# Kernel tuning notes

Hardware: AMD Instinct MI355X
Metric: run time of the kernel (lower is better)

## Reference

```python
import jax, jax.numpy as jnp
import numpy as np


def setup_inputs() -> dict:
    key = jax.random.key(0)
    B, T, D, H = 32, 2048, 128, 256
    ks = jax.random.split(key, 13)
    s_in = 1.0 / np.sqrt(D)
    s_h = 1.0 / np.sqrt(H)
    return {
        "x": jax.random.normal(ks[0], (B, T, D), jnp.float32),
        "wf": jax.random.normal(ks[1], (D, H), jnp.float32) * s_in,
        "wi": jax.random.normal(ks[2], (D, H), jnp.float32) * s_in,
        "wo": jax.random.normal(ks[3], (D, H), jnp.float32) * s_in,
        "wc": jax.random.normal(ks[4], (D, H), jnp.float32) * s_in,
        "uf": jax.random.normal(ks[5], (H, H), jnp.float32) * s_h,
        "ui": jax.random.normal(ks[6], (H, H), jnp.float32) * s_h,
        "uo": jax.random.normal(ks[7], (H, H), jnp.float32) * s_h,
        "uc": jax.random.normal(ks[8], (H, H), jnp.float32) * s_h,
        "bf": jax.random.normal(ks[9], (1, H), jnp.float32) * 0.01,
        "bi": jax.random.normal(ks[10], (1, H), jnp.float32) * 0.01,
        "bo": jax.random.normal(ks[11], (1, H), jnp.float32) * 0.01,
        "bc": jax.random.normal(ks[12], (1, H), jnp.float32) * 0.01,
    }


def reference(x, wf, wi, wo, wc, uf, ui, uo, uc, bf, bi, bo, bc):
    # Standard 4-gate LSTM over time, matching the per-gate weights of myLSTM.
    # Fuse the four input projections into one GEMM over all timesteps up front
    # (same math as per-step x_t @ w*), then scan the recurrence.
    B, T, D = x.shape
    H = wf.shape[1]
    W = jnp.concatenate([wf, wi, wo, wc], axis=1)            # [D, 4H]
    U = jnp.concatenate([uf, ui, uo, uc], axis=1)            # [H, 4H]
    b = jnp.concatenate([bf, bi, bo, bc], axis=1)            # [1, 4H]
    xg = jnp.einsum('btd,dg->btg', x, W) + b                 # [B, T, 4H]
    xg = jnp.swapaxes(xg, 0, 1)                              # [T, B, 4H]

    def step(carry, xg_t):
        h, c = carry
        g = xg_t + h @ U                                     # [B, 4H]
        f = jax.nn.sigmoid(g[:, 0 * H:1 * H])
        i = jax.nn.sigmoid(g[:, 1 * H:2 * H])
        o = jax.nn.sigmoid(g[:, 2 * H:3 * H])
        cand = jnp.tanh(g[:, 3 * H:4 * H])
        c_new = f * c + i * cand
        h_new = o * jnp.tanh(c_new)
        return (h_new, c_new), h_new

    h0 = jnp.zeros((B, H), x.dtype)
    c0 = jnp.zeros((B, H), x.dtype)
    (_, _), hs = jax.lax.scan(step, (h0, c0), xg)            # hs: [T, B, H]
    return jnp.swapaxes(hs, 0, 1)                            # [B, T, H]
```

## Files before the change

### kernel.cpp

```cpp
#include <hip/hip_runtime.h>
#include <hip/hip_fp16.h>
#include <cstdint>

#define BB 32
#define TT 2048
#define DD 128
#define HH 256

typedef _Float16 half2v __attribute__((ext_vector_type(2)));
typedef uint32_t u32x4 __attribute__((ext_vector_type(4)));

__device__ inline float dot2f16(uint32_t a, uint32_t b, float c) {
#if __has_builtin(__builtin_amdgcn_fdot2)
  half2v ah = __builtin_bit_cast(half2v, a);
  half2v bh = __builtin_bit_cast(half2v, b);
  return __builtin_amdgcn_fdot2(ah, bh, c, false);
#else
  float d;
  asm("v_dot2_f32_f16 %0, %1, %2, %3" : "=v"(d) : "v"(a), "v"(b), "v"(c));
  return d;
#endif
}

__device__ inline float fsigmoid(float x) { return __frcp_rn(1.f + __expf(-x)); }
__device__ inline float ftanh_(float x)   { return 1.f - 2.f * __frcp_rn(1.f + __expf(2.f * x)); }


__global__ void repack_u3_kernel(const float* __restrict__ uf, const float* __restrict__ ui_,
                                 const float* __restrict__ uo, const float* __restrict__ uc,
                                 __half* __restrict__ Ut) {
  int idx = blockIdx.x * 256 + threadIdx.x;
  int cg = idx >> 12;
  int rem = idx & 4095;
  int j = rem >> 3, r = rem & 7;
  int a = cg >> 3, c = cg & 7;
  int nn = a >> 2, g = a & 3;
  int s = j & 3, u = j >> 2;
  int n = 2 * u + nn;
  int k = s * 64 + c * 8 + r;
  const float* U[4] = {uf, ui_, uo, uc};
  Ut[idx] = __float2half(U[g][k * HH + n]);
}

__global__ void repack_w2_kernel(const float* __restrict__ wf, const float* __restrict__ wi,
                                 const float* __restrict__ wo, const float* __restrict__ wc,
                                 const float* __restrict__ bf, const float* __restrict__ bi,
                                 const float* __restrict__ bo, const float* __restrict__ bc,
                                 __half* __restrict__ Wt, float* __restrict__ bs) {
  int idx = blockIdx.x * 256 + threadIdx.x;
  int m = idx >> 7, k = idx & 127;
  int g = m & 3, n = m >> 2;
  const float* W[4] = {wf, wi, wo, wc};
  Wt[idx] = __float2half(W[g][k * HH + n]);
  if (idx < 1024) {
    const float* B[4] = {bf, bi, bo, bc};
    bs[idx] = B[idx & 3][idx >> 2];
  }
}

__global__ __launch_bounds__(256, 4) void xg_gemm_kernel(
    const float* __restrict__ x, const __half* __restrict__ Wt,
    const float* __restrict__ bs, __half* __restrict__ xg) {
  __shared__ __align__(16) __half As[64][136];
  __shared__ __align__(16) __half Bs[64][136];
  const int tid = threadIdx.x;
  const int r0 = (blockIdx.x >> 4) * 64;
  const int m0 = (blockIdx.x & 15) * 64;

#pragma unroll
  for (int it = 0; it < 8; ++it) {
    int fi = it * 256 + tid;
    int row = fi >> 5, col4 = fi & 31;
    float4 v = ((const float4*)(x + (size_t)(r0 + row) * DD))[col4];
    __half2 lo; lo.x = __float2half(v.x); lo.y = __float2half(v.y);
    __half2 hi; hi.x = __float2half(v.z); hi.y = __float2half(v.w);
    uint2 pk; pk.x = __builtin_bit_cast(uint32_t, lo); pk.y = __builtin_bit_cast(uint32_t, hi);
    *(uint2*)&As[row][col4 * 4] = pk;
  }
#pragma unroll
  for (int it = 0; it < 4; ++it) {
    int ui = it * 256 + tid;
    int row = ui >> 4, c16 = ui & 15;
    uint4 v = ((const uint4*)(Wt + (size_t)(m0 + row) * DD))[c16];
    *(uint4*)&Bs[row][c16 * 8] = v;
  }
  __syncthreads();

  const int ty = tid >> 4, tx = tid & 15;
  float acc[4][4] = {};
#pragma unroll
  for (int kc = 0; kc < 16; ++kc) {
    uint4 av[4], bv[4];
#pragma unroll
    for (int d = 0; d < 4; ++d) {
      av[d] = *(const uint4*)&As[ty * 4 + d][kc * 8];
      bv[d] = *(const uint4*)&Bs[tx * 4 + d][kc * 8];
    }
#pragma unroll
    for (int di = 0; di < 4; ++di)
#pragma unroll
      for (int dj = 0; dj < 4; ++dj) {
        acc[di][dj] = dot2f16(av[di].x, bv[dj].x, acc[di][dj]);
        acc[di][dj] = dot2f16(av[di].y, bv[dj].y, acc[di][dj]);
        acc[di][dj] = dot2f16(av[di].z, bv[dj].z, acc[di][dj]);
        acc[di][dj] = dot2f16(av[di].w, bv[dj].w, acc[di][dj]);
      }
  }

#pragma unroll
  for (int di = 0; di < 4; ++di) {
    const int grow = r0 + ty * 4 + di;
    __half2 o01, o23;
    o01.x = __float2half(acc[di][0] + bs[m0 + tx * 4 + 0]);
    o01.y = __float2half(acc[di][1] + bs[m0 + tx * 4 + 1]);
    o23.x = __float2half(acc[di][2] + bs[m0 + tx * 4 + 2]);
    o23.y = __float2half(acc[di][3] + bs[m0 + tx * 4 + 3]);
    uint2 pk; pk.x = __builtin_bit_cast(uint32_t, o01); pk.y = __builtin_bit_cast(uint32_t, o23);
    *(uint2*)&xg[(size_t)grow * 1024 + m0 + tx * 4] = pk;
  }
}

__global__ __launch_bounds__(512, 1) void lstm5_kernel(
    const __half* __restrict__ Ut, const __half* __restrict__ xg,
    float* __restrict__ out) {
  __shared__ __align__(16) __half Ul[16 * 512 * 8];
  __shared__ __align__(16) __half hl[2][4][72];

  const int j = threadIdx.x;
  const int b = blockIdx.x;
  const int s = j & 3, u = j >> 2;
  const int nsel = 2 * u + (s & 1);

  const __half* xgb = xg + (size_t)b * TT * 1024;
  float* ob = out + (size_t)b * TT * HH;

#pragma unroll
  for (int a = 0; a < 8; ++a)
#pragma unroll
    for (int c6 = 0; c6 < 2; ++c6) {
      uint4 v = *(const uint4*)(Ut + ((size_t)(a * 8 + 6 + c6) * 512 + j) * 8);
      *(uint4*)(Ul + ((size_t)(a * 2 + c6) * 512 + j) * 8) = v;
    }

  u32x4 R[48];
#pragma unroll
  for (int a = 0; a < 8; ++a)
#pragma unroll
    for (int c = 0; c < 6; ++c) {
      const void* p = (const char*)Ut + (((size_t)(a * 8 + c) * 512 + j) * 16);
      asm volatile("global_load_dwordx4 %0, %1, off"
                   : "=v"(R[a * 6 + c]) : "v"(p));
    }
  asm volatile("s_waitcnt vmcnt(0)" ::: "memory");

  if (j < HH) hl[0][j >> 6][j & 63] = __float2half(0.f);

  uint2 xgc = *(const uint2*)(xgb + (size_t)nsel * 4);
  float cst = 0.f;
  int cur = 0;

  for (int t = 0; t < TT; ++t) {
    const int nxt = cur ^ 1;
    const int tn = (t + 1 < TT) ? (t + 1) : t;
    const uint2 xgn = *(const uint2*)(xgb + (size_t)tn * 1024 + (size_t)nsel * 4);

    asm volatile("s_waitcnt lgkmcnt(0)" ::: "memory");
    __builtin_amdgcn_s_barrier();

    const __half* hrow = &hl[cur][s][0];
    float acc[8] = {0.f, 0.f, 0.f, 0.f, 0.f, 0.f, 0.f, 0.f};

#pragma unroll
    for (int c = 0; c < 6; ++c) {
      const uint4 hq = *(const uint4*)(hrow + c * 8);
#pragma unroll
      for (int a = 0; a < 8; ++a) {
        const u32x4 uv = R[a * 6 + c];
        acc[a] = dot2f16(uv[0], hq.x, acc[a]);
        acc[a] = dot2f16(uv[1], hq.y, acc[a]);
        acc[a] = dot2f16(uv[2], hq.z, acc[a]);
        acc[a] = dot2f16(uv[3], hq.w, acc[a]);
      }
    }
#pragma unroll
    for (int c6 = 0; c6 < 2; ++c6) {
      const uint4 hq = *(const uint4*)(hrow + (6 + c6) * 8);
#pragma unroll
      for (int a = 0; a < 8; ++a) {
        const uint4 uv = *(const uint4*)(Ul + ((size_t)(a * 2 + c6) * 512 + j) * 8);
        acc[a] = dot2f16(uv.x, hq.x, acc[a]);
        acc[a] = dot2f16(uv.y, hq.y, acc[a]);
        acc[a] = dot2f16(uv.z, hq.z, acc[a]);
        acc[a] = dot2f16(uv.w, hq.w, acc[a]);
      }
    }

#pragma unroll
    for (int a = 0; a < 8; ++a) {
      acc[a] += __shfl_xor(acc[a], 1);
      acc[a] += __shfl_xor(acc[a], 2);
    }

    const int hiSel = s & 1;
    const float af = hiSel ? acc[4] : acc[0];
    const float ai = hiSel ? acc[5] : acc[1];
    const float ao = hiSel ? acc[6] : acc[2];
    const float ac = hiSel ? acc[7] : acc[3];

    const __half2 x01 = __builtin_bit_cast(__half2, xgc.x);
    const __half2 x23 = __builtin_bit_cast(__half2, xgc.y);
    const float gf = fsigmoid(af + __half2float(x01.x));
    const float gi = fsigmoid(ai + __half2float(x01.y));
    const float go = fsigmoid(ao + __half2float(x23.x));
    const float cd = ftanh_(ac + __half2float(x23.y));
    cst = gf * cst + gi * cd;
    const float hv = go * ftanh_(cst);

    uint32_t hb = (uint32_t)__half_as_ushort(__float2half(hv));
    uint32_t pb = (uint32_t)__shfl_xor((int)hb, 1);
    if (s == 0) {
      *(uint32_t*)&hl[nxt][nsel >> 6][nsel & 63] = hb | (pb << 16);
    }
    if (s < 2) ob[(size_t)t * HH + nsel] = hv;

    xgc = xgn;
    cur = nxt;
  }
}


__global__ void repack_kernel(const float* __restrict__ wf, const float* __restrict__ wi,
                              const float* __restrict__ wo, const float* __restrict__ wc,
                              const float* __restrict__ uf, const float* __restrict__ ui,
                              const float* __restrict__ uo, const float* __restrict__ uc,
                              __half* __restrict__ Vt) {
  int idx = blockIdx.x * 256 + threadIdx.x;
  int gq = idx >> 13;
  int g = gq / 12;
  int q = gq - g * 12;
  int rem = idx & 8191;
  int jj = rem >> 3;
  int r = rem & 7;
  int n = jj >> 2;
  int s = jj & 3;
  int k = s * 96 + q * 8 + r;
  const float* Wg[4] = {wf, wi, wo, wc};
  const float* Ug[4] = {uf, ui, uo, uc};
  float v = (k < DD) ? Wg[g][k * HH + n] : Ug[g][(k - DD) * HH + n];
  Vt[idx] = __float2half(v);
}

__global__ __launch_bounds__(1024, 4) void lstm_kernel(
    const float* __restrict__ x, const __half* __restrict__ Vt,
    const float* __restrict__ bf, const float* __restrict__ bi,
    const float* __restrict__ bo, const float* __restrict__ bc,
    float* __restrict__ out) {
  __shared__ __align__(16) __half hx[2][384];
  const int j = threadIdx.x;
  const int b = blockIdx.x;
  const int n = j >> 2;
  const int s = j & 3;
  const float* xb = x + (size_t)b * TT * DD;
  float* ob = out + (size_t)b * TT * HH;
  const float bias_f = bf[n], bias_i = bi[n], bias_o = bo[n], bias_c = bc[n];

  if (j < HH) hx[0][DD + j] = __float2half(0.f);
  if (j < 32) {
    float4 xa = ((const float4*)xb)[j];
    __half2* dst = (__half2*)hx[0];
    __half2 p0q; p0q.x = __float2half(xa.x); p0q.y = __float2half(xa.y);
    __half2 p1q; p1q.x = __float2half(xa.z); p1q.y = __float2half(xa.w);
    dst[2 * j] = p0q; dst[2 * j + 1] = p1q;
  }
  float c = 0.f;
  const uint4* vbase = (const uint4*)Vt + j;
  int cur = 0;
  for (int t = 0; t < TT; ++t) {
    const int nxt = cur ^ 1;
    __syncthreads();
    if (j < 32 && t + 1 < TT) {
      float4 xa = ((const float4*)(xb + (size_t)(t + 1) * DD))[j];
      __half2* dst = (__half2*)hx[nxt];
      __half2 p0q; p0q.x = __float2half(xa.x); p0q.y = __float2half(xa.y);
      __half2 p1q; p1q.x = __float2half(xa.z); p1q.y = __float2half(xa.w);
      dst[2 * j] = p0q; dst[2 * j + 1] = p1q;
    }
    float af = 0.f, ai = 0.f, ao = 0.f, ac = 0.f;
    const uint4* hp = (const uint4*)(&hx[cur][s * 96]);
#pragma unroll 4
    for (int q = 0; q < 12; ++q) {
      uint4 hq = hp[q];
      uint4 v0 = vbase[(0 * 12 + q) * 1024];
      uint4 v1 = vbase[(1 * 12 + q) * 1024];
      uint4 v2 = vbase[(2 * 12 + q) * 1024];
      uint4 v3 = vbase[(3 * 12 + q) * 1024];
      af = dot2f16(v0.x, hq.x, af); af = dot2f16(v0.y, hq.y, af);
      af = dot2f16(v0.z, hq.z, af); af = dot2f16(v0.w, hq.w, af);
      ai = dot2f16(v1.x, hq.x, ai); ai = dot2f16(v1.y, hq.y, ai);
      ai = dot2f16(v1.z, hq.z, ai); ai = dot2f16(v1.w, hq.w, ai);
      ao = dot2f16(v2.x, hq.x, ao); ao = dot2f16(v2.y, hq.y, ao);
      ao = dot2f16(v2.z, hq.z, ao); ao = dot2f16(v2.w, hq.w, ao);
      ac = dot2f16(v3.x, hq.x, ac); ac = dot2f16(v3.y, hq.y, ac);
      ac = dot2f16(v3.z, hq.z, ac); ac = dot2f16(v3.w, hq.w, ac);
    }
    af += __shfl_xor(af, 1); af += __shfl_xor(af, 2);
    ai += __shfl_xor(ai, 1); ai += __shfl_xor(ai, 2);
    ao += __shfl_xor(ao, 1); ao += __shfl_xor(ao, 2);
    ac += __shfl_xor(ac, 1); ac += __shfl_xor(ac, 2);
    float fg = fsigmoid(af + bias_f);
    float ig = fsigmoid(ai + bias_i);
    float og = fsigmoid(ao + bias_o);
    float cd = ftanh_(ac + bias_c);
    c = fg * c + ig * cd;
    float hv = og * ftanh_(c);
    if (s == 0) {
      hx[nxt][DD + n] = __float2half(hv);
      ob[(size_t)t * HH + n] = hv;
    }
    cur = nxt;
  }
}


extern "C" void kernel_launch(void* const* d_in, const int* in_sizes, int n_in,
                              void* d_out, int out_size, void* d_ws, size_t ws_size,
                              hipStream_t stream) {
  const float* x  = (const float*)d_in[0];
  const float* wf = (const float*)d_in[1];
  const float* wi = (const float*)d_in[2];
  const float* wo = (const float*)d_in[3];
  const float* wc = (const float*)d_in[4];
  const float* uf = (const float*)d_in[5];
  const float* ui = (const float*)d_in[6];
  const float* uo = (const float*)d_in[7];
  const float* uc = (const float*)d_in[8];
  const float* bf = (const float*)d_in[9];
  const float* bi = (const float*)d_in[10];
  const float* bo = (const float*)d_in[11];
  const float* bc = (const float*)d_in[12];

  const size_t UT_OFF = 0;
  const size_t WT_OFF = 524288;
  const size_t BS_OFF = 786432;
  const size_t XG_OFF = 790528;
  const size_t NEED = XG_OFF + (size_t)BB * TT * 1024 * 2;

  if (ws_size >= NEED) {
    __half* Ut = (__half*)((char*)d_ws + UT_OFF);
    __half* Wt = (__half*)((char*)d_ws + WT_OFF);
    float*  bs = (float*)((char*)d_ws + BS_OFF);
    __half* xg = (__half*)((char*)d_ws + XG_OFF);

    repack_u3_kernel<<<1024, 256, 0, stream>>>(uf, ui, uo, uc, Ut);
    repack_w2_kernel<<<512, 256, 0, stream>>>(wf, wi, wo, wc, bf, bi, bo, bc, Wt, bs);
    xg_gemm_kernel<<<16384, 256, 0, stream>>>(x, Wt, bs, xg);
    lstm5_kernel<<<BB, 512, 0, stream>>>(Ut, xg, (float*)d_out);
  } else {
    __half* Vt = (__half*)d_ws;
    repack_kernel<<<1536, 256, 0, stream>>>(wf, wi, wo, wc, uf, ui, uo, uc, Vt);
    lstm_kernel<<<BB, 1024, 0, stream>>>(x, Vt, bf, bi, bo, bc, (float*)d_out);
  }
}
```

Baseline: 4.115 ms.

## Stream most recurrent weights from global per step instead of holding in registers

Restructures the recurrent LSTM kernel so only 5 weight slices stay in registers and 19 in shared memory. The remaining 40 slices are reloaded from global memory each timestep in staggered batches interleaved with the dot-product work. The weight repack order changes to match, and launch bounds allow two blocks per CU. This is meant to cut register pressure. In exchange it adds heavy per-step global/L2 traffic and load latency on the serial recurrence.

```diff
diff --git a/kernel.cpp b/kernel.cpp
--- a/kernel.cpp
+++ b/kernel.cpp
@@ -22,18 +22,33 @@
 #endif
 }
 
+__device__ inline float dot4q(const u32x4 uv, const uint4 hq, float a) {
+  a = dot2f16(uv[0], hq.x, a);
+  a = dot2f16(uv[1], hq.y, a);
+  a = dot2f16(uv[2], hq.z, a);
+  a = dot2f16(uv[3], hq.w, a);
+  return a;
+}
+__device__ inline float dot4u(const uint4 uv, const uint4 hq, float a) {
+  a = dot2f16(uv.x, hq.x, a);
+  a = dot2f16(uv.y, hq.y, a);
+  a = dot2f16(uv.z, hq.z, a);
+  a = dot2f16(uv.w, hq.w, a);
+  return a;
+}
+
 __device__ inline float fsigmoid(float x) { return __frcp_rn(1.f + __expf(-x)); }
 __device__ inline float ftanh_(float x)   { return 1.f - 2.f * __frcp_rn(1.f + __expf(2.f * x)); }
 
 
-__global__ void repack_u3_kernel(const float* __restrict__ uf, const float* __restrict__ ui_,
+__global__ void repack_u7_kernel(const float* __restrict__ uf, const float* __restrict__ ui_,
                                  const float* __restrict__ uo, const float* __restrict__ uc,
                                  __half* __restrict__ Ut) {
   int idx = blockIdx.x * 256 + threadIdx.x;
-  int cg = idx >> 12;
+  int sid = idx >> 12;
   int rem = idx & 4095;
   int j = rem >> 3, r = rem & 7;
-  int a = cg >> 3, c = cg & 7;
+  int c = sid >> 3, a = sid & 7;
   int nn = a >> 2, g = a & 3;
   int s = j & 3, u = j >> 2;
   int n = 2 * u + nn;
@@ -120,10 +135,13 @@
   }
 }
 
-__global__ __launch_bounds__(512, 1) void lstm5_kernel(
+#define ULD(sid) (*(const uint4*)(Ul + ((size_t)(sid) * 512 + j) * 8))
+#define SLD(sid) (*(const uint4*)(Ut + ((size_t)(sid) * 512 + j) * 8))
+
+__global__ __launch_bounds__(512, 2) void lstm11_kernel(
     const __half* __restrict__ Ut, const __half* __restrict__ xg,
     float* __restrict__ out) {
-  __shared__ __align__(16) __half Ul[16 * 512 * 8];
+  __shared__ __align__(16) __half Ul[19 * 512 * 8];
   __shared__ __align__(16) __half hl[2][4][72];
 
   const int j = threadIdx.x;
@@ -135,22 +153,17 @@
   float* ob = out + (size_t)b * TT * HH;
 
 #pragma unroll
-  for (int a = 0; a < 8; ++a)
-#pragma unroll
-    for (int c6 = 0; c6 < 2; ++c6) {
-      uint4 v = *(const uint4*)(Ut + ((size_t)(a * 8 + 6 + c6) * 512 + j) * 8);
-      *(uint4*)(Ul + ((size_t)(a * 2 + c6) * 512 + j) * 8) = v;
-    }
-
-  u32x4 R[48];
-#pragma unroll
-  for (int a = 0; a < 8; ++a)
-#pragma unroll
-    for (int c = 0; c < 6; ++c) {
-      const void* p = (const char*)Ut + (((size_t)(a * 8 + c) * 512 + j) * 16);
-      asm volatile("global_load_dwordx4 %0, %1, off"
-                   : "=v"(R[a * 6 + c]) : "v"(p));
-    }
+  for (int sid = 0; sid < 19; ++sid) {
+    uint4 v = SLD(sid);
+    *(uint4*)(Ul + ((size_t)sid * 512 + j) * 8) = v;
+  }
+
+  u32x4 R[5];
+#pragma unroll
+  for (int i = 0; i < 5; ++i) {
+    const void* p = (const char*)Ut + (((size_t)(19 + i) * 512 + j) * 16);
+    asm volatile("global_load_dwordx4 %0, %1, off" : "=v"(R[i]) : "v"(p));
+  }
   asm volatile("s_waitcnt vmcnt(0)" ::: "memory");
 
   if (j < HH) hl[0][j >> 6][j & 63] = __float2half(0.f);
@@ -162,6 +175,10 @@
   for (int t = 0; t < TT; ++t) {
     const int nxt = cur ^ 1;
     const int tn = (t + 1 < TT) ? (t + 1) : t;
+
+    uint4 SA[8];
+#pragma unroll
+    for (int i = 0; i < 8; ++i) SA[i] = SLD(24 + i);
     const uint2 xgn = *(const uint2*)(xgb + (size_t)tn * 1024 + (size_t)nsel * 4);
 
     asm volatile("s_waitcnt lgkmcnt(0)" ::: "memory");
@@ -169,31 +186,58 @@
 
     const __half* hrow = &hl[cur][s][0];
     float acc[8] = {0.f, 0.f, 0.f, 0.f, 0.f, 0.f, 0.f, 0.f};
-
-#pragma unroll
-    for (int c = 0; c < 6; ++c) {
-      const uint4 hq = *(const uint4*)(hrow + c * 8);
-#pragma unroll
-      for (int a = 0; a < 8; ++a) {
-        const u32x4 uv = R[a * 6 + c];
-        acc[a] = dot2f16(uv[0], hq.x, acc[a]);
-        acc[a] = dot2f16(uv[1], hq.y, acc[a]);
-        acc[a] = dot2f16(uv[2], hq.z, acc[a]);
-        acc[a] = dot2f16(uv[3], hq.w, acc[a]);
-      }
-    }
-#pragma unroll
-    for (int c6 = 0; c6 < 2; ++c6) {
-      const uint4 hq = *(const uint4*)(hrow + (6 + c6) * 8);
-#pragma unroll
-      for (int a = 0; a < 8; ++a) {
-        const uint4 uv = *(const uint4*)(Ul + ((size_t)(a * 2 + c6) * 512 + j) * 8);
-        acc[a] = dot2f16(uv.x, hq.x, acc[a]);
-        acc[a] = dot2f16(uv.y, hq.y, acc[a]);
-        acc[a] = dot2f16(uv.z, hq.z, acc[a]);
-        acc[a] = dot2f16(uv.w, hq.w, acc[a]);
-      }
-    }
+    uint4 hq;
+
+    hq = *(const uint4*)(hrow + 0);
+#pragma unroll
+    for (int a = 0; a < 8; ++a) acc[a] = dot4u(ULD(a), hq, acc[a]);
+
+    uint4 SB[8];
+#pragma unroll
+    for (int i = 0; i < 8; ++i) SB[i] = SLD(32 + i);
+
+    hq = *(const uint4*)(hrow + 8);
+#pragma unroll
+    for (int a = 0; a < 8; ++a) acc[a] = dot4u(ULD(8 + a), hq, acc[a]);
+
+    hq = *(const uint4*)(hrow + 24);
+#pragma unroll
+    for (int a = 0; a < 8; ++a) acc[a] = dot4u(SA[a], hq, acc[a]);
+
+    uint4 SC[8];
+#pragma unroll
+    for (int i = 0; i < 8; ++i) SC[i] = SLD(40 + i);
+
+    hq = *(const uint4*)(hrow + 16);
+    acc[0] = dot4u(ULD(16), hq, acc[0]);
+    acc[1] = dot4u(ULD(17), hq, acc[1]);
+    acc[2] = dot4u(ULD(18), hq, acc[2]);
+#pragma unroll
+    for (int i = 0; i < 5; ++i) acc[3 + i] = dot4q(R[i], hq, acc[3 + i]);
+
+    hq = *(const uint4*)(hrow + 32);
+#pragma unroll
+    for (int a = 0; a < 8; ++a) acc[a] = dot4u(SB[a], hq, acc[a]);
+
+    uint4 SD[8];
+#pragma unroll
+    for (int i = 0; i < 8; ++i) SD[i] = SLD(48 + i);
+
+    hq = *(const uint4*)(hrow + 40);
+#pragma unroll
+    for (int a = 0; a < 8; ++a) acc[a] = dot4u(SC[a], hq, acc[a]);
+
+    uint4 SE[8];
+#pragma unroll
+    for (int i = 0; i < 8; ++i) SE[i] = SLD(56 + i);
+
+    hq = *(const uint4*)(hrow + 48);
+#pragma unroll
+    for (int a = 0; a < 8; ++a) acc[a] = dot4u(SD[a], hq, acc[a]);
+
+    hq = *(const uint4*)(hrow + 56);
+#pragma unroll
+    for (int a = 0; a < 8; ++a) acc[a] = dot4u(SE[a], hq, acc[a]);
 
 #pragma unroll
     for (int a = 0; a < 8; ++a) {
@@ -240,10 +284,10 @@
   int q = gq - g * 12;
   int rem = idx & 8191;
   int jj = rem >> 3;
-  int r = rem & 7;
+  int rr = rem & 7;
   int n = jj >> 2;
   int s = jj & 3;
-  int k = s * 96 + q * 8 + r;
+  int k = s * 96 + q * 8 + rr;
   const float* Wg[4] = {wf, wi, wo, wc};
   const float* Ug[4] = {uf, ui, uo, uc};
   float v = (k < DD) ? Wg[g][k * HH + n] : Ug[g][(k - DD) * HH + n];
@@ -351,10 +395,10 @@
     float*  bs = (float*)((char*)d_ws + BS_OFF);
     __half* xg = (__half*)((char*)d_ws + XG_OFF);
 
-    repack_u3_kernel<<<1024, 256, 0, stream>>>(uf, ui, uo, uc, Ut);
+    repack_u7_kernel<<<1024, 256, 0, stream>>>(uf, ui, uo, uc, Ut);
     repack_w2_kernel<<<512, 256, 0, stream>>>(wf, wi, wo, wc, bf, bi, bo, bc, Wt, bs);
     xg_gemm_kernel<<<16384, 256, 0, stream>>>(x, Wt, bs, xg);
-    lstm5_kernel<<<BB, 512, 0, stream>>>(Ut, xg, (float*)d_out);
+    lstm11_kernel<<<BB, 512, 0, stream>>>(Ut, xg, (float*)d_out);
   } else {
     __half* Vt = (__half*)d_ws;
     repack_kernel<<<1536, 256, 0, stream>>>(wf, wi, wo, wc, uf, ui, uo, uc, Vt);
```

Result: slower. 6.548 ms (+59.1%).
